# Kernel tuning notes

Measured on AMD Instinct MI355X. Metric: run time of the kernel, lower is better.

The kernel has to match this reference:

```python
import jax, jax.numpy as jnp
import numpy as np

N = 100000          # number of nodes (src == dst in this sampled graph)
DEG = 8             # uniform sampled fan-in (max_num_neighbors)
E = N * DEG         # number of edges
IN_C = 128
HEADS = 4
OUT_C = 32
NEG_SLOPE = 0.2


def setup_inputs() -> dict:
    key = jax.random.key(0)
    k1, k2, k3, k4, k5 = jax.random.split(key, 5)
    x = jax.random.normal(k1, (N, IN_C), dtype=jnp.float32)
    csr_row_ptr = jnp.arange(N + 1, dtype=jnp.int64) * DEG
    csr_col_ind = jax.random.randint(k2, (E,), 0, N, dtype=jnp.int64)
    # learned params (xavier-normal-ish scaling)
    lin_w = jax.random.normal(k3, (IN_C, HEADS * OUT_C), dtype=jnp.float32) * np.sqrt(2.0 / (IN_C + HEADS * OUT_C))
    att = jax.random.normal(k4, (2 * HEADS * OUT_C,), dtype=jnp.float32) * np.sqrt(2.0 / (1 + OUT_C))
    bias = jnp.zeros((HEADS * OUT_C,), dtype=jnp.float32)
    return {"x": x, "csr_row_ptr": csr_row_ptr, "csr_col_ind": csr_col_ind,
            "max_num_neighbors": DEG, "lin_w": lin_w, "att": att, "bias": bias}


def reference(x, csr_row_ptr, csr_col_ind, max_num_neighbors, lin_w, att, bias):
    n = x.shape[0]
    e = csr_col_ind.shape[0]
    hc = HEADS * OUT_C
    # linear projection: [N, H, C]
    xp = (x @ lin_w).reshape(n, HEADS, OUT_C)
    att_src = att[:hc].reshape(HEADS, OUT_C)
    att_dst = att[hc:].reshape(HEADS, OUT_C)
    # per-node attention logits per head: [N, H]
    a_src = jnp.einsum('nhc,hc->nh', xp, att_src)
    a_dst = jnp.einsum('nhc,hc->nh', xp, att_dst)
    # expand CSR row_ptr into per-edge destination ids: [E]
    dst = jnp.searchsorted(csr_row_ptr, jnp.arange(e, dtype=csr_row_ptr.dtype), side='right') - 1
    src = csr_col_ind
    # edge scores + per-destination softmax over incoming edges
    logits = jax.nn.leaky_relu(a_src[src] + a_dst[dst], NEG_SLOPE)  # [E, H]
    m = jax.ops.segment_max(logits, dst, num_segments=n)            # [N, H]
    ex = jnp.exp(logits - m[dst])
    denom = jax.ops.segment_sum(ex, dst, num_segments=n)            # [N, H]
    alpha = ex / denom[dst]                                         # [E, H]
    # weighted aggregation of neighbor features: [N, H, C]
    out = jax.ops.segment_sum(alpha[:, :, None] * xp[src], dst, num_segments=n)
    out = out.reshape(n, hc) + bias  # concat=True
    return out
```

## Files before the change

### kernel.cpp

```cpp
#include <hip/hip_runtime.h>
#include <stdint.h>

#define HEADS 4
#define NEG_SLOPE 0.2f
#define MB 64

typedef _Float16 f16;
typedef f16 f16x8 __attribute__((ext_vector_type(8)));
typedef f16 f16x4 __attribute__((ext_vector_type(4)));
typedef float f32x4 __attribute__((ext_vector_type(4)));
typedef unsigned int u32x4 __attribute__((ext_vector_type(4)));

#define SWZ(row, kb) (((row) << 8) + ((kb) ^ (((row) & 7) << 4)))

__global__ __launch_bounds__(256) void wt_kernel(const float* __restrict__ w,
                                                 f16* __restrict__ wt) {
    __shared__ f16 tl[16][136];
    const int b = blockIdx.x, t = threadIdx.x;
    for (int i = t; i < 2048; i += 256) {
        int k = i >> 4, nl = i & 15;
        tl[nl][k] = (f16)w[k * 128 + b * 16 + nl];
    }
    __syncthreads();
    {
        int nl = t >> 4, kc = t & 15;
        f16x8 v = *(const f16x8*)&tl[nl][kc * 8];
        *(f16x8*)(wt + (b * 16 + nl) * 128 + kc * 8) = v;
    }
}

__global__ __launch_bounds__(256) void gat_proj_mfma(
    const float* __restrict__ x, const f16* __restrict__ wt,
    const float* __restrict__ att, f16* __restrict__ xp,
    float* __restrict__ a_src, float* __restrict__ a_dst, int n) {
    __shared__ unsigned char lds[32768];
    __shared__ float att_l[256];
    const int t = threadIdx.x;
    const int node0 = blockIdx.x * MB;
    const int lane = t & 63;
    const int wv = t >> 6;

    att_l[t] = att[t];

    const int arow = node0 + wv * 16 + (lane & 15);
    const bool rowok = arow < n;
    const float* xr = x + (size_t)arow * 128 + (lane >> 4) * 8;
    f16x8 afr[4];
#pragma unroll
    for (int kt = 0; kt < 4; kt++) {
        float4 a = make_float4(0.f, 0.f, 0.f, 0.f), b = a;
        if (rowok) {
            a = *(const float4*)(xr + kt * 32);
            b = *(const float4*)(xr + kt * 32 + 4);
        }
        f16x8 hv;
        hv[0] = (f16)a.x; hv[1] = (f16)a.y; hv[2] = (f16)a.z; hv[3] = (f16)a.w;
        hv[4] = (f16)b.x; hv[5] = (f16)b.y; hv[6] = (f16)b.z; hv[7] = (f16)b.w;
        afr[kt] = hv;
    }

    for (int i = t; i < 2048; i += 256) {
        int row = i >> 4, kc = i & 15;
        uint4 v = *(const uint4*)(wt + row * 128 + kc * 8);
        *(uint4*)(lds + SWZ(row, kc * 16)) = v;
    }
    __syncthreads();

    f32x4 acc[8];
#pragma unroll
    for (int nf = 0; nf < 8; nf++) acc[nf] = (f32x4){0.f, 0.f, 0.f, 0.f};

#pragma unroll
    for (int kt = 0; kt < 4; kt++) {
        const int kb = kt * 64 + (lane >> 4) * 16;
#pragma unroll
        for (int nf = 0; nf < 8; nf++) {
            f16x8 bfr = *(const f16x8*)(lds + SWZ(nf * 16 + (lane & 15), kb));
            acc[nf] = __builtin_amdgcn_mfma_f32_16x16x32_f16(afr[kt], bfr, acc[nf], 0, 0, 0);
        }
    }

    __syncthreads();
#pragma unroll
    for (int r = 0; r < 4; r++) {
        int row = wv * 16 + (lane >> 4) * 4 + r;
#pragma unroll
        for (int nf = 0; nf < 8; nf++) {
            int col = nf * 16 + (lane & 15);
            *(f16*)(lds + SWZ(row, col * 2)) = (f16)acc[nf][r];
        }
    }
    __syncthreads();

    {
        int row = t >> 2, h = t & 3;
        int grow = node0 + row;
        if (grow < n) {
            float s = 0.f, d = 0.f;
#pragma unroll
            for (int cc = 0; cc < 4; cc++) {
                f16x8 v = *(const f16x8*)(lds + SWZ(row, h * 64 + cc * 16));
#pragma unroll
                for (int j = 0; j < 8; j++) {
                    float xv = (float)v[j];
                    int c = cc * 8 + j;
                    s = fmaf(xv, att_l[h * 32 + c], s);
                    d = fmaf(xv, att_l[128 + h * 32 + c], d);
                }
            }
            a_src[(size_t)grow * HEADS + h] = s;
            a_dst[(size_t)grow * HEADS + h] = d;
        }
    }
    for (int i = t; i < 1024; i += 256) {
        int row = i >> 4, kc = i & 15;
        int grow = node0 + row;
        if (grow < n) {
            u32x4 v = *(const u32x4*)(lds + SWZ(row, kc * 16));
            __builtin_nontemporal_store(v, (u32x4*)(xp + (size_t)grow * 128 + kc * 8));
        }
    }
}

__global__ __launch_bounds__(256) void gat_aggr_kernel(
    const f16* __restrict__ xp, const float* __restrict__ a_src,
    const float* __restrict__ a_dst, const int* __restrict__ row_ptr,
    const int* __restrict__ col_ind, const float* __restrict__ bias,
    float* __restrict__ out, int n, int e_total) {
    const int lane = threadIdx.x & 63;
    const int p = lane >> 5, l = lane & 31;
    const int nb = (blockIdx.x * 4 + (threadIdx.x >> 6)) * 4;
    if (nb >= n) return;

    int rp = 0;
    if (lane < 5) {
        int idx = nb + lane;
        if (idx > n) idx = n;
        rp = row_ptr[idx];
    }
    int ci = 0;
    {
        int si = nb * 8 + lane;
        if (lane < 32 && si < e_total) ci = col_ind[si];
    }
    float4 b4 = ((const float4*)bias)[l];

    int rs0 = __shfl(rp, 0, 64), rs1 = __shfl(rp, 1, 64), rs2 = __shfl(rp, 2, 64);
    int rs3 = __shfl(rp, 3, 64), rs4 = __shfl(rp, 4, 64);
    int dg0 = rs1 - rs0, dg1 = rs2 - rs1, dg2 = rs3 - rs2, dg3 = rs4 - rs3;
    if (dg0 > 8) dg0 = 8;
    if (dg1 > 8) dg1 = 8;
    if (dg2 > 8) dg2 = 8;
    if (dg3 > 8) dg3 = 8;
    if (nb + 1 >= n) dg1 = 0;
    if (nb + 2 >= n) dg2 = 0;
    if (nb + 3 >= n) dg3 = 0;
    bool ok = (nb + 4 <= n) && (rs0 == nb * 8) && (rs1 == rs0 + 8) &&
              (rs2 == rs1 + 8) && (rs3 == rs2 + 8) && (rs4 == rs3 + 8);
    if (!ok) {
        int j = lane >> 3, e = lane & 7;
        int rsj = (j == 0) ? rs0 : (j == 1) ? rs1 : (j == 2) ? rs2 : rs3;
        int dgj = (j == 0) ? dg0 : (j == 1) ? dg1 : (j == 2) ? dg2 : dg3;
        int v = 0;
        if (lane < 32 && e < dgj) v = col_ind[rsj + e];
        ci = v;
    }

    f16x4 pv[16];
#pragma unroll
    for (int k = 0; k < 16; k++) {
        int j = k >> 2, e = 2 * (k & 3) + p;
        int s = __shfl(ci, j * 8 + e, 64);
        pv[k] = *(const f16x4*)(xp + (size_t)s * 128 + l * 4);
    }

    const int ea = (l >> 2) & 7, ha = l & 3;
    const int dsel0 = p ? dg1 : dg0;
    const int dsel1 = p ? dg3 : dg2;
    int sa0 = __shfl(ci, (0 * 2 + p) * 8 + ea, 64);
    int sa1 = __shfl(ci, (1 * 2 + p) * 8 + ea, 64);
    float av0 = (ea < dsel0) ? a_src[(size_t)sa0 * HEADS + ha] : 0.f;
    float av1 = (ea < dsel1) ? a_src[(size_t)sa1 * HEADS + ha] : 0.f;
    float dv0 = (nb + p < n) ? a_dst[(size_t)(nb + p) * HEADS + ha] : 0.f;
    float dv1 = (nb + 2 + p < n) ? a_dst[(size_t)(nb + 2 + p) * HEADS + ha] : 0.f;

    float alpha[2];
#pragma unroll
    for (int q = 0; q < 2; q++) {
        const int dsel = q ? dsel1 : dsel0;
        float z = (q ? av1 : av0) + (q ? dv1 : dv0);
        float v = (ea < dsel) ? ((z >= 0.f) ? z : NEG_SLOPE * z) : -1e30f;
        float m = v;
        m = fmaxf(m, __shfl_xor(m, 4, 64));
        m = fmaxf(m, __shfl_xor(m, 8, 64));
        m = fmaxf(m, __shfl_xor(m, 16, 64));
        float ex = (ea < dsel) ? __expf(v - m) : 0.f;
        float ss = ex;
        ss += __shfl_xor(ss, 4, 64);
        ss += __shfl_xor(ss, 8, 64);
        ss += __shfl_xor(ss, 16, 64);
        alpha[q] = ex * ((ss > 0.f) ? (1.f / ss) : 0.f);
    }

    const int h = l >> 3;
    float acc[4][4] = {{0.f, 0.f, 0.f, 0.f}, {0.f, 0.f, 0.f, 0.f},
                       {0.f, 0.f, 0.f, 0.f}, {0.f, 0.f, 0.f, 0.f}};
#pragma unroll
    for (int k = 0; k < 16; k++) {
        const int j = k >> 2;
        int e = 2 * (k & 3) + p;
        float a = __shfl(alpha[j >> 1], (j & 1) * 32 + e * 4 + h, 64);
        f16x4 pvv = pv[k];
        acc[j][0] = fmaf(a, (float)pvv[0], acc[j][0]);
        acc[j][1] = fmaf(a, (float)pvv[1], acc[j][1]);
        acc[j][2] = fmaf(a, (float)pvv[2], acc[j][2]);
        acc[j][3] = fmaf(a, (float)pvv[3], acc[j][3]);
    }
#pragma unroll
    for (int j = 0; j < 4; j++)
#pragma unroll
        for (int c = 0; c < 4; c++)
            acc[j][c] += __shfl_xor(acc[j][c], 32, 64);

#pragma unroll
    for (int q = 0; q < 2; q++) {
        int j = 2 * q + p;
        if (nb + j < n) {
            f32x4 o;
            o[0] = (p ? acc[2 * q + 1][0] : acc[2 * q][0]) + b4.x;
            o[1] = (p ? acc[2 * q + 1][1] : acc[2 * q][1]) + b4.y;
            o[2] = (p ? acc[2 * q + 1][2] : acc[2 * q][2]) + b4.z;
            o[3] = (p ? acc[2 * q + 1][3] : acc[2 * q][3]) + b4.w;
            __builtin_nontemporal_store(o, (f32x4*)(out + (size_t)(nb + j) * 128 + l * 4));
        }
    }
}

extern "C" void kernel_launch(void* const* d_in, const int* in_sizes, int n_in,
                              void* d_out, int out_size, void* d_ws, size_t ws_size,
                              hipStream_t stream) {
    const float* x = (const float*)d_in[0];
    const int* row_ptr = (const int*)d_in[1];
    const int* col_ind = (const int*)d_in[2];
    const float* lin_w = (const float*)d_in[4];
    const float* att = (const float*)d_in[5];
    const float* bias = (const float*)d_in[6];
    float* out = (float*)d_out;
    const int n = in_sizes[0] / 128;
    const int e_total = in_sizes[2];

    f16* xp = (f16*)d_ws;
    float* a_src = (float*)((char*)d_ws + (size_t)n * 128 * 2);
    float* a_dst = a_src + (size_t)n * HEADS;
    f16* wt = (f16*)(a_dst + (size_t)n * HEADS);

    hipLaunchKernelGGL(wt_kernel, dim3(8), dim3(256), 0, stream, lin_w, wt);
    hipLaunchKernelGGL(gat_proj_mfma, dim3((n + MB - 1) / MB), dim3(256), 0, stream,
                       x, wt, att, xp, a_src, a_dst, n);
    hipLaunchKernelGGL(gat_aggr_kernel, dim3((n + 15) / 16), dim3(256), 0, stream,
                       xp, a_src, a_dst, row_ptr, col_ind, bias, out, n, e_total);
}
```

Measured before the change: 69.42 us.

## Recompute source attention logits from gathered features instead of storing a_src

```diff
diff --git a/kernel.cpp b/kernel.cpp
--- a/kernel.cpp
+++ b/kernel.cpp
@@ -32,15 +32,15 @@
 __global__ __launch_bounds__(256) void gat_proj_mfma(
     const float* __restrict__ x, const f16* __restrict__ wt,
     const float* __restrict__ att, f16* __restrict__ xp,
-    float* __restrict__ a_src, float* __restrict__ a_dst, int n) {
+    float* __restrict__ a_dst, int n) {
     __shared__ unsigned char lds[32768];
-    __shared__ float att_l[256];
+    __shared__ float att_l[128];
     const int t = threadIdx.x;
     const int node0 = blockIdx.x * MB;
     const int lane = t & 63;
     const int wv = t >> 6;
 
-    att_l[t] = att[t];
+    if (t < 128) att_l[t] = att[128 + t];
 
     const int arow = node0 + wv * 16 + (lane & 15);
     const bool rowok = arow < n;
@@ -96,19 +96,14 @@
         int row = t >> 2, h = t & 3;
         int grow = node0 + row;
         if (grow < n) {
-            float s = 0.f, d = 0.f;
+            float d = 0.f;
 #pragma unroll
             for (int cc = 0; cc < 4; cc++) {
                 f16x8 v = *(const f16x8*)(lds + SWZ(row, h * 64 + cc * 16));
 #pragma unroll
-                for (int j = 0; j < 8; j++) {
-                    float xv = (float)v[j];
-                    int c = cc * 8 + j;
-                    s = fmaf(xv, att_l[h * 32 + c], s);
-                    d = fmaf(xv, att_l[128 + h * 32 + c], d);
-                }
+                for (int j = 0; j < 8; j++)
+                    d = fmaf((float)v[j], att_l[h * 32 + cc * 8 + j], d);
             }
-            a_src[(size_t)grow * HEADS + h] = s;
             a_dst[(size_t)grow * HEADS + h] = d;
         }
     }
@@ -123,7 +118,7 @@
 }
 
 __global__ __launch_bounds__(256) void gat_aggr_kernel(
-    const f16* __restrict__ xp, const float* __restrict__ a_src,
+    const f16* __restrict__ xp, const float* __restrict__ att,
     const float* __restrict__ a_dst, const int* __restrict__ row_ptr,
     const int* __restrict__ col_ind, const float* __restrict__ bias,
     float* __restrict__ out, int n, int e_total) {
@@ -142,6 +137,12 @@
     {
         int si = nb * 8 + lane;
         if (lane < 32 && si < e_total) ci = col_ind[si];
+    }
+    float4 att4 = ((const float4*)att)[l];
+    float adv = 0.f;
+    {
+        int idx = nb + (lane >> 2);
+        if (lane < 16 && idx < n) adv = a_dst[(size_t)idx * HEADS + (lane & 3)];
     }
     float4 b4 = ((const float4*)bias)[l];
 
@@ -174,63 +175,74 @@
         pv[k] = *(const f16x4*)(xp + (size_t)s * 128 + l * 4);
     }
 
-    const int ea = (l >> 2) & 7, ha = l & 3;
-    const int dsel0 = p ? dg1 : dg0;
-    const int dsel1 = p ? dg3 : dg2;
-    int sa0 = __shfl(ci, (0 * 2 + p) * 8 + ea, 64);
-    int sa1 = __shfl(ci, (1 * 2 + p) * 8 + ea, 64);
-    float av0 = (ea < dsel0) ? a_src[(size_t)sa0 * HEADS + ha] : 0.f;
-    float av1 = (ea < dsel1) ? a_src[(size_t)sa1 * HEADS + ha] : 0.f;
-    float dv0 = (nb + p < n) ? a_dst[(size_t)(nb + p) * HEADS + ha] : 0.f;
-    float dv1 = (nb + 2 + p < n) ? a_dst[(size_t)(nb + 2 + p) * HEADS + ha] : 0.f;
-
-    float alpha[2];
-#pragma unroll
-    for (int q = 0; q < 2; q++) {
-        const int dsel = q ? dsel1 : dsel0;
-        float z = (q ? av1 : av0) + (q ? dv1 : dv0);
-        float v = (ea < dsel) ? ((z >= 0.f) ? z : NEG_SLOPE * z) : -1e30f;
-        float m = v;
-        m = fmaxf(m, __shfl_xor(m, 4, 64));
-        m = fmaxf(m, __shfl_xor(m, 8, 64));
-        m = fmaxf(m, __shfl_xor(m, 16, 64));
-        float ex = (ea < dsel) ? __expf(v - m) : 0.f;
-        float ss = ex;
-        ss += __shfl_xor(ss, 4, 64);
-        ss += __shfl_xor(ss, 8, 64);
-        ss += __shfl_xor(ss, 16, 64);
-        alpha[q] = ex * ((ss > 0.f) ? (1.f / ss) : 0.f);
-    }
+    float zown[16];
+#pragma unroll
+    for (int k = 0; k < 16; k++) {
+        float d = fmaf((float)pv[k][0], att4.x,
+                  fmaf((float)pv[k][1], att4.y,
+                  fmaf((float)pv[k][2], att4.z,
+                       (float)pv[k][3] * att4.w)));
+        d += __shfl_xor(d, 1, 64);
+        d += __shfl_xor(d, 2, 64);
+        d += __shfl_xor(d, 4, 64);
+        zown[k] = d;
+    }
+    float zoth[16];
+#pragma unroll
+    for (int k = 0; k < 16; k++) zoth[k] = __shfl_xor(zown[k], 32, 64);
 
     const int h = l >> 3;
-    float acc[4][4] = {{0.f, 0.f, 0.f, 0.f}, {0.f, 0.f, 0.f, 0.f},
-                       {0.f, 0.f, 0.f, 0.f}, {0.f, 0.f, 0.f, 0.f}};
-#pragma unroll
-    for (int k = 0; k < 16; k++) {
-        const int j = k >> 2;
-        int e = 2 * (k & 3) + p;
-        float a = __shfl(alpha[j >> 1], (j & 1) * 32 + e * 4 + h, 64);
-        f16x4 pvv = pv[k];
-        acc[j][0] = fmaf(a, (float)pvv[0], acc[j][0]);
-        acc[j][1] = fmaf(a, (float)pvv[1], acc[j][1]);
-        acc[j][2] = fmaf(a, (float)pvv[2], acc[j][2]);
-        acc[j][3] = fmaf(a, (float)pvv[3], acc[j][3]);
+    float accv[4][4] = {{0.f, 0.f, 0.f, 0.f}, {0.f, 0.f, 0.f, 0.f},
+                        {0.f, 0.f, 0.f, 0.f}, {0.f, 0.f, 0.f, 0.f}};
+#pragma unroll
+    for (int j = 0; j < 4; j++) {
+        const int dgj = (j == 0) ? dg0 : (j == 1) ? dg1 : (j == 2) ? dg2 : dg3;
+        float ad = __shfl(adv, j * 4 + h, 64);
+        float l1[4], l2[4];
+#pragma unroll
+        for (int m = 0; m < 4; m++) {
+            float z1 = zown[4 * j + m] + ad;
+            z1 = (z1 >= 0.f) ? z1 : NEG_SLOPE * z1;
+            l1[m] = ((2 * m + p) < dgj) ? z1 : -1e30f;
+            float z2 = zoth[4 * j + m] + ad;
+            z2 = (z2 >= 0.f) ? z2 : NEG_SLOPE * z2;
+            l2[m] = ((2 * m + (1 - p)) < dgj) ? z2 : -1e30f;
+        }
+        float mx = fmaxf(fmaxf(fmaxf(l1[0], l1[1]), fmaxf(l1[2], l1[3])),
+                         fmaxf(fmaxf(l2[0], l2[1]), fmaxf(l2[2], l2[3])));
+        float e1[4], ss = 0.f;
+#pragma unroll
+        for (int m = 0; m < 4; m++) {
+            e1[m] = __expf(l1[m] - mx);
+            ss += e1[m];
+            ss += __expf(l2[m] - mx);
+        }
+        float inv = 1.f / ss;
+#pragma unroll
+        for (int m = 0; m < 4; m++) {
+            float a = e1[m] * inv;
+            f16x4 pvv = pv[4 * j + m];
+            accv[j][0] = fmaf(a, (float)pvv[0], accv[j][0]);
+            accv[j][1] = fmaf(a, (float)pvv[1], accv[j][1]);
+            accv[j][2] = fmaf(a, (float)pvv[2], accv[j][2]);
+            accv[j][3] = fmaf(a, (float)pvv[3], accv[j][3]);
+        }
     }
 #pragma unroll
     for (int j = 0; j < 4; j++)
 #pragma unroll
         for (int c = 0; c < 4; c++)
-            acc[j][c] += __shfl_xor(acc[j][c], 32, 64);
+            accv[j][c] += __shfl_xor(accv[j][c], 32, 64);
 
 #pragma unroll
     for (int q = 0; q < 2; q++) {
         int j = 2 * q + p;
         if (nb + j < n) {
             f32x4 o;
-            o[0] = (p ? acc[2 * q + 1][0] : acc[2 * q][0]) + b4.x;
-            o[1] = (p ? acc[2 * q + 1][1] : acc[2 * q][1]) + b4.y;
-            o[2] = (p ? acc[2 * q + 1][2] : acc[2 * q][2]) + b4.z;
-            o[3] = (p ? acc[2 * q + 1][3] : acc[2 * q][3]) + b4.w;
+            o[0] = (p ? accv[2 * q + 1][0] : accv[2 * q][0]) + b4.x;
+            o[1] = (p ? accv[2 * q + 1][1] : accv[2 * q][1]) + b4.y;
+            o[2] = (p ? accv[2 * q + 1][2] : accv[2 * q][2]) + b4.z;
+            o[3] = (p ? accv[2 * q + 1][3] : accv[2 * q][3]) + b4.w;
             __builtin_nontemporal_store(o, (f32x4*)(out + (size_t)(nb + j) * 128 + l * 4));
         }
     }
@@ -250,13 +262,12 @@
     const int e_total = in_sizes[2];
 
     f16* xp = (f16*)d_ws;
-    float* a_src = (float*)((char*)d_ws + (size_t)n * 128 * 2);
-    float* a_dst = a_src + (size_t)n * HEADS;
+    float* a_dst = (float*)((char*)d_ws + (size_t)n * 128 * 2);
     f16* wt = (f16*)(a_dst + (size_t)n * HEADS);
 
     hipLaunchKernelGGL(wt_kernel, dim3(8), dim3(256), 0, stream, lin_w, wt);
     hipLaunchKernelGGL(gat_proj_mfma, dim3((n + MB - 1) / MB), dim3(256), 0, stream,
-                       x, wt, att, xp, a_src, a_dst, n);
+                       x, wt, att, xp, a_dst, n);
     hipLaunchKernelGGL(gat_aggr_kernel, dim3((n + 15) / 16), dim3(256), 0, stream,
-                       xp, a_src, a_dst, row_ptr, col_ind, bias, out, n, e_total);
-}
+                       xp, att, a_dst, row_ptr, col_ind, bias, out, n, e_total);
+}
```

Result: no change. 69.45 us (+0.0%).

## Split aggregation into alpha kernel and channel-sliced gather over sliced xp layout

Applied to the files above, without the earlier changes.

```diff
diff --git a/kernel.cpp b/kernel.cpp
--- a/kernel.cpp
+++ b/kernel.cpp
@@ -8,6 +8,7 @@
 typedef _Float16 f16;
 typedef f16 f16x8 __attribute__((ext_vector_type(8)));
 typedef f16 f16x4 __attribute__((ext_vector_type(4)));
+typedef f16 f16x2 __attribute__((ext_vector_type(2)));
 typedef float f32x4 __attribute__((ext_vector_type(4)));
 typedef unsigned int u32x4 __attribute__((ext_vector_type(4)));
 
@@ -117,16 +118,16 @@
         int grow = node0 + row;
         if (grow < n) {
             u32x4 v = *(const u32x4*)(lds + SWZ(row, kc * 16));
-            __builtin_nontemporal_store(v, (u32x4*)(xp + (size_t)grow * 128 + kc * 8));
-        }
-    }
-}
-
-__global__ __launch_bounds__(256) void gat_aggr_kernel(
-    const f16* __restrict__ xp, const float* __restrict__ a_src,
-    const float* __restrict__ a_dst, const int* __restrict__ row_ptr,
-    const int* __restrict__ col_ind, const float* __restrict__ bias,
-    float* __restrict__ out, int n, int e_total) {
+            int slice = kc >> 1;
+            *(u32x4*)(xp + ((size_t)slice * n + grow) * 16 + (kc & 1) * 8) = v;
+        }
+    }
+}
+
+__global__ __launch_bounds__(256) void gat_alpha_kernel(
+    const float* __restrict__ a_src, const float* __restrict__ a_dst,
+    const int* __restrict__ row_ptr, const int* __restrict__ col_ind,
+    f16* __restrict__ alpha, int n, int e_total) {
     const int lane = threadIdx.x & 63;
     const int p = lane >> 5, l = lane & 31;
     const int nb = (blockIdx.x * 4 + (threadIdx.x >> 6)) * 4;
@@ -143,7 +144,6 @@
         int si = nb * 8 + lane;
         if (lane < 32 && si < e_total) ci = col_ind[si];
     }
-    float4 b4 = ((const float4*)bias)[l];
 
     int rs0 = __shfl(rp, 0, 64), rs1 = __shfl(rp, 1, 64), rs2 = __shfl(rp, 2, 64);
     int rs3 = __shfl(rp, 3, 64), rs4 = __shfl(rp, 4, 64);
@@ -166,14 +166,6 @@
         ci = v;
     }
 
-    f16x4 pv[16];
-#pragma unroll
-    for (int k = 0; k < 16; k++) {
-        int j = k >> 2, e = 2 * (k & 3) + p;
-        int s = __shfl(ci, j * 8 + e, 64);
-        pv[k] = *(const f16x4*)(xp + (size_t)s * 128 + l * 4);
-    }
-
     const int ea = (l >> 2) & 7, ha = l & 3;
     const int dsel0 = p ? dg1 : dg0;
     const int dsel1 = p ? dg3 : dg2;
@@ -184,9 +176,9 @@
     float dv0 = (nb + p < n) ? a_dst[(size_t)(nb + p) * HEADS + ha] : 0.f;
     float dv1 = (nb + 2 + p < n) ? a_dst[(size_t)(nb + 2 + p) * HEADS + ha] : 0.f;
 
-    float alpha[2];
 #pragma unroll
     for (int q = 0; q < 2; q++) {
+        const int node = nb + 2 * q + p;
         const int dsel = q ? dsel1 : dsel0;
         float z = (q ? av1 : av0) + (q ? dv1 : dv0);
         float v = (ea < dsel) ? ((z >= 0.f) ? z : NEG_SLOPE * z) : -1e30f;
@@ -199,40 +191,80 @@
         ss += __shfl_xor(ss, 4, 64);
         ss += __shfl_xor(ss, 8, 64);
         ss += __shfl_xor(ss, 16, 64);
-        alpha[q] = ex * ((ss > 0.f) ? (1.f / ss) : 0.f);
-    }
-
-    const int h = l >> 3;
-    float acc[4][4] = {{0.f, 0.f, 0.f, 0.f}, {0.f, 0.f, 0.f, 0.f},
-                       {0.f, 0.f, 0.f, 0.f}, {0.f, 0.f, 0.f, 0.f}};
-#pragma unroll
-    for (int k = 0; k < 16; k++) {
-        const int j = k >> 2;
-        int e = 2 * (k & 3) + p;
-        float a = __shfl(alpha[j >> 1], (j & 1) * 32 + e * 4 + h, 64);
-        f16x4 pvv = pv[k];
-        acc[j][0] = fmaf(a, (float)pvv[0], acc[j][0]);
-        acc[j][1] = fmaf(a, (float)pvv[1], acc[j][1]);
-        acc[j][2] = fmaf(a, (float)pvv[2], acc[j][2]);
-        acc[j][3] = fmaf(a, (float)pvv[3], acc[j][3]);
-    }
-#pragma unroll
-    for (int j = 0; j < 4; j++)
-#pragma unroll
-        for (int c = 0; c < 4; c++)
-            acc[j][c] += __shfl_xor(acc[j][c], 32, 64);
-
-#pragma unroll
-    for (int q = 0; q < 2; q++) {
-        int j = 2 * q + p;
-        if (nb + j < n) {
-            f32x4 o;
-            o[0] = (p ? acc[2 * q + 1][0] : acc[2 * q][0]) + b4.x;
-            o[1] = (p ? acc[2 * q + 1][1] : acc[2 * q][1]) + b4.y;
-            o[2] = (p ? acc[2 * q + 1][2] : acc[2 * q][2]) + b4.z;
-            o[3] = (p ? acc[2 * q + 1][3] : acc[2 * q][3]) + b4.w;
-            __builtin_nontemporal_store(o, (f32x4*)(out + (size_t)(nb + j) * 128 + l * 4));
-        }
+        float al = ex * ((ss > 0.f) ? (1.f / ss) : 0.f);
+        if (node < n)
+            alpha[(size_t)ha * n * 8 + (size_t)node * 8 + ea] = (f16)al;
+    }
+}
+
+__global__ __launch_bounds__(256) void gat_slice_aggr(
+    const f16* __restrict__ xp, const f16* __restrict__ alpha,
+    const int* __restrict__ row_ptr, const int* __restrict__ col_ind,
+    const float* __restrict__ bias, float* __restrict__ out, int n, int e_total) {
+    const int slice = blockIdx.x & 7;
+    const int chunk = blockIdx.x >> 3;
+    const int lane = threadIdx.x & 63;
+    const int nb = chunk * 32 + (threadIdx.x >> 6) * 8;
+    if (nb >= n) return;
+
+    const f16* xps = xp + (size_t)slice * n * 16;
+    const f16* alp = alpha + (size_t)(slice >> 1) * n * 8;
+
+    int rp = 0;
+    if (lane < 9) {
+        int idx = nb + lane;
+        if (idx > n) idx = n;
+        rp = row_ptr[idx];
+    }
+    int ci = 0;
+    {
+        long long si = (long long)nb * 8 + lane;
+        if (si < e_total) ci = col_ind[si];
+    }
+    int avi = 0;
+    {
+        long long ai = (long long)nb * 8 + lane;
+        if (ai < (long long)n * 8) avi = *(const unsigned short*)(alp + ai);
+    }
+    const int e = lane >> 3, c2 = lane & 7;
+    float2 b2 = *(const float2*)(bias + slice * 16 + c2 * 2);
+
+    bool ok = __all((lane < 9) ? (rp == (nb + lane) * 8) : 1) && (nb + 8 <= n);
+
+    float sto0 = 0.f, sto1 = 0.f;
+#pragma unroll
+    for (int nd = 0; nd < 8; nd++) {
+        int src, abits;
+        if (ok) {
+            src = __shfl(ci, nd * 8 + e, 64);
+            abits = __shfl(avi, nd * 8 + e, 64);
+        } else {
+            int rs = __shfl(rp, nd, 64), re = __shfl(rp, nd + 1, 64);
+            int dg = re - rs;
+            if (dg > 8) dg = 8;
+            if (nb + nd >= n) dg = 0;
+            src = (e < dg) ? col_ind[rs + e] : 0;
+            abits = (nb + nd < n) ? *(const unsigned short*)(alp + (size_t)(nb + nd) * 8 + e) : 0;
+        }
+        unsigned short ab16 = (unsigned short)abits;
+        float a = (float)(*(const f16*)&ab16);
+        f16x2 v = *(const f16x2*)(xps + (size_t)src * 16 + c2 * 2);
+        float p0 = a * (float)v[0];
+        float p1 = a * (float)v[1];
+        p0 += __shfl_xor(p0, 8, 64);
+        p1 += __shfl_xor(p1, 8, 64);
+        p0 += __shfl_xor(p0, 16, 64);
+        p1 += __shfl_xor(p1, 16, 64);
+        p0 += __shfl_xor(p0, 32, 64);
+        p1 += __shfl_xor(p1, 32, 64);
+        sto0 = (nd == e) ? p0 : sto0;
+        sto1 = (nd == e) ? p1 : sto1;
+    }
+    const int snode = nb + e;
+    if (snode < n) {
+        float2 o = make_float2(sto0 + b2.x, sto1 + b2.y);
+        __builtin_nontemporal_store(o.x, out + (size_t)snode * 128 + slice * 16 + c2 * 2);
+        __builtin_nontemporal_store(o.y, out + (size_t)snode * 128 + slice * 16 + c2 * 2 + 1);
     }
 }
 
@@ -250,13 +282,16 @@
     const int e_total = in_sizes[2];
 
     f16* xp = (f16*)d_ws;
-    float* a_src = (float*)((char*)d_ws + (size_t)n * 128 * 2);
+    float* a_src = (float*)((char*)d_ws + (size_t)n * 256);
     float* a_dst = a_src + (size_t)n * HEADS;
-    f16* wt = (f16*)(a_dst + (size_t)n * HEADS);
+    f16* alpha = (f16*)(a_dst + (size_t)n * HEADS);
+    f16* wt = alpha + (size_t)n * 32 + 128;
 
     hipLaunchKernelGGL(wt_kernel, dim3(8), dim3(256), 0, stream, lin_w, wt);
     hipLaunchKernelGGL(gat_proj_mfma, dim3((n + MB - 1) / MB), dim3(256), 0, stream,
                        x, wt, att, xp, a_src, a_dst, n);
-    hipLaunchKernelGGL(gat_aggr_kernel, dim3((n + 15) / 16), dim3(256), 0, stream,
-                       xp, a_src, a_dst, row_ptr, col_ind, bias, out, n, e_total);
-}
+    hipLaunchKernelGGL(gat_alpha_kernel, dim3((n + 15) / 16), dim3(256), 0, stream,
+                       a_src, a_dst, row_ptr, col_ind, alpha, n, e_total);
+    hipLaunchKernelGGL(gat_slice_aggr, dim3(8 * ((n + 31) / 32)), dim3(256), 0, stream,
+                       xp, alpha, row_ptr, col_ind, bias, out, n, e_total);
+}
```

Result: slower. 111.1 us (+60.0%).
